# Performance work log

Measured on AMD Instinct MI355X. Metric: run time of the kernel, lower is better.

Reference implementation:

```python
import jax, jax.numpy as jnp
import numpy as np

N_NODES = 100000
N_EDGES = 1600000
N_FEAT = 128
HIDDEN = 128
N_CLASSES = 40


def gcn_conv(x, W, b, src, dst, norm, n):
    # PyG GCNConv: linear (no bias) -> gather src -> scale by sym norm -> scatter-add to dst -> + bias
    h = x @ W                      # [N, out]
    m = h[src] * norm[:, None]     # [E+N, out] gathered, normalized messages
    out = jax.ops.segment_sum(m, dst, num_segments=n)
    return out + b


def setup_inputs() -> dict:
    key = jax.random.key(0)
    ks = jax.random.split(key, 10)
    x = jax.random.normal(ks[0], (N_NODES, N_FEAT), dtype=jnp.float32)
    edge_index = jax.random.randint(ks[1], (2, N_EDGES), 0, N_NODES, dtype=jnp.int32)

    def lin(k, fan_in, fan_out):
        s = 1.0 / np.sqrt(fan_in)
        return (jax.random.uniform(k, (fan_in, fan_out), jnp.float32, -s, s))

    return {
        "x": x,
        "edge_index": edge_index,
        "W1": lin(ks[2], N_FEAT, HIDDEN), "b1": jnp.zeros((HIDDEN,), jnp.float32),
        "W2": lin(ks[3], HIDDEN, HIDDEN), "b2": jnp.zeros((HIDDEN,), jnp.float32),
        "W3": lin(ks[4], HIDDEN, HIDDEN), "b3": jnp.zeros((HIDDEN,), jnp.float32),
        "W4": lin(ks[5], HIDDEN, N_CLASSES), "b4": jnp.zeros((N_CLASSES,), jnp.float32),
    }


def reference(x, edge_index, W1, b1, W2, b2, W3, b3, W4, b4):
    n = x.shape[0]
    # add self-loops (PyG GCNConv default)
    loops = jnp.arange(n, dtype=edge_index.dtype)
    src = jnp.concatenate([edge_index[0], loops])
    dst = jnp.concatenate([edge_index[1], loops])
    # symmetric degree normalization: deg computed on destination index
    deg = jax.ops.segment_sum(jnp.ones_like(dst, x.dtype), dst, num_segments=n)
    dinv = jnp.where(deg > 0, jax.lax.rsqrt(deg), 0.0)
    norm = dinv[src] * dinv[dst]

    h = jax.nn.relu(gcn_conv(x, W1, b1, src, dst, norm, n))   # dropout = identity (eval)
    h = jax.nn.relu(gcn_conv(h, W2, b2, src, dst, norm, n))
    h = jax.nn.relu(gcn_conv(h, W3, b3, src, dst, norm, n))
    x_latent = h
    out = gcn_conv(h, W4, b4, src, dst, norm, n)
    return out, x_latent
```

## Files before the change

### kernel.cpp

```cpp
#include <hip/hip_runtime.h>
#include <hip/hip_bf16.h>
#include <hip/hip_fp16.h>


#define N_NODES 100000
#define N_EDGES 1600000

#define BSHIFT 7
#define BWIDTH 128
#define CELL_CAP 512
#define P1_EPT 16
#define P1_CHUNK 4096

typedef short s16x8 __attribute__((ext_vector_type(8)));
typedef _Float16 f16x8 __attribute__((ext_vector_type(8)));
typedef float f32x4 __attribute__((ext_vector_type(4)));
typedef float f32x2 __attribute__((ext_vector_type(2)));


__global__ __launch_bounds__(256) void pass1_bucket(const int* __restrict__ src,
                                                    const int* __restrict__ dst,
                                                    int* __restrict__ bcur2,
                                                    int2* __restrict__ cells,
                                                    int2* __restrict__ spill,
                                                    int* __restrict__ spillCnt,
                                                    int nb, int e) {
    __shared__ int hist[1024];
    __shared__ int base[1024];
    int t = threadIdx.x;
    int x = blockIdx.x & 7;
    int e0 = blockIdx.x * P1_CHUNK;

    for (int i = t; i < nb; i += 256) hist[i] = 0;
    __syncthreads();

    int ds[P1_EPT], ss[P1_EPT];
#pragma unroll
    for (int j = 0; j < P1_EPT; j++) {
        int i = e0 + j * 256 + t;
        if (i < e) {
            ds[j] = dst[i];
            ss[j] = src[i];
            atomicAdd(&hist[ds[j] >> BSHIFT], 1);
        } else {
            ds[j] = -1;
        }
    }
    __syncthreads();

    for (int i = t; i < nb; i += 256) {
        int h = hist[i];
        base[i] = (h > 0) ? atomicAdd(&bcur2[i * 8 + x], h) : 0;
        hist[i] = 0;
    }
    __syncthreads();

#pragma unroll
    for (int j = 0; j < P1_EPT; j++) {
        if (ds[j] >= 0) {
            int b = ds[j] >> BSHIFT;
            int r = atomicAdd(&hist[b], 1);
            int slot = base[b] + r;
            if (slot < CELL_CAP) {
                cells[(size_t)(b * 8 + x) * CELL_CAP + slot] = make_int2(ss[j], ds[j]);
            } else {
                int sp = atomicAdd(spillCnt, 1);
                spill[sp] = make_int2(ss[j], ds[j]);
            }
        }
    }
}

__global__ __launch_bounds__(256) void count_cells(const int* __restrict__ bcur2,
                                                   const int2* __restrict__ cells,
                                                   const int2* __restrict__ spill,
                                                   const int* __restrict__ spillCnt,
                                                   int* __restrict__ counts,
                                                   float* __restrict__ dinv,
                                                   int n) {
    __shared__ int cnt[BWIDTH];
    int b = blockIdx.x;
    int t = threadIdx.x;
    int nodeBase = b << BSHIFT;
    if (t < BWIDTH) cnt[t] = 0;
    __syncthreads();
    for (int x = 0; x < 8; x++) {
        int c = bcur2[b * 8 + x];
        if (c > CELL_CAP) c = CELL_CAP;
        const int2* cp = cells + (size_t)(b * 8 + x) * CELL_CAP;
        for (int s = t; s < c; s += 256) {
            atomicAdd(&cnt[cp[s].y - nodeBase], 1);
        }
    }
    int sc = *spillCnt;
    for (int s = t; s < sc; s += 256) {
        int d = spill[s].y;
        if ((d >> BSHIFT) == b) atomicAdd(&cnt[d - nodeBase], 1);
    }
    __syncthreads();
    if (t < BWIDTH) {
        int node = nodeBase + t;
        if (node < n) {
            int deg = cnt[t] + 1;
            counts[node] = deg;
            dinv[node] = 1.0f / sqrtf((float)deg);
        }
    }
}

__global__ __launch_bounds__(256) void scan_phase1(const int* __restrict__ counts,
                                                   int* __restrict__ blockSums, int n) {
    __shared__ int red[256];
    int t = threadIdx.x;
    int base = blockIdx.x * 1024 + t * 4;
    int s = 0;
    if (base + 3 < n) {
        int4 v = *(const int4*)(counts + base);
        s = ((v.x + 2) & ~3) + ((v.y + 2) & ~3) + ((v.z + 2) & ~3) + ((v.w + 2) & ~3);
    } else {
        for (int j = 0; j < 4; j++) if (base + j < n) s += (counts[base + j] + 2) & ~3;
    }
    red[t] = s;
    __syncthreads();
    for (int off = 128; off > 0; off >>= 1) {
        if (t < off) red[t] += red[t + off];
        __syncthreads();
    }
    if (t == 0) blockSums[blockIdx.x] = red[0];
}

__global__ __launch_bounds__(1024) void scan_phase2(int* __restrict__ blockSums, int nb) {
    __shared__ int sh[1024];
    int t = threadIdx.x;
    sh[t] = (t < nb) ? blockSums[t] : 0;
    __syncthreads();
    for (int off = 1; off < 1024; off <<= 1) {
        int v = (t >= off) ? sh[t - off] : 0;
        __syncthreads();
        sh[t] += v;
        __syncthreads();
    }
    if (t < nb) blockSums[t] = (t == 0) ? 0 : sh[t - 1];
}

__global__ __launch_bounds__(256) void scan_phase3(const int* __restrict__ counts,
                                                   const int* __restrict__ blockSums,
                                                   int* __restrict__ offsets, int n) {
    __shared__ int red[256];
    int t = threadIdx.x;
    int base = blockIdx.x * 1024 + t * 4;
    int c[4];
#pragma unroll
    for (int j = 0; j < 4; j++) c[j] = (base + j < n) ? ((counts[base + j] + 2) & ~3) : 0;
    int s = c[0] + c[1] + c[2] + c[3];
    red[t] = s;
    __syncthreads();
    for (int off = 1; off < 256; off <<= 1) {
        int v = (t >= off) ? red[t - off] : 0;
        __syncthreads();
        red[t] += v;
        __syncthreads();
    }
    int prefix = blockSums[blockIdx.x] + ((t == 0) ? 0 : red[t - 1]);
#pragma unroll
    for (int j = 0; j < 4; j++) {
        if (base + j < n) offsets[base + j] = prefix;
        prefix += c[j];
        if (base + j == n - 1) offsets[n] = prefix;
    }
}

__global__ __launch_bounds__(256) void pass2_scatter(const int* __restrict__ bcur2,
                                                     const int2* __restrict__ cells,
                                                     const int2* __restrict__ spill,
                                                     const int* __restrict__ spillCnt,
                                                     const int* __restrict__ offsets,
                                                     int* __restrict__ srcSorted, int n) {
    __shared__ int cur[BWIDTH];
    int b = blockIdx.x;
    int t = threadIdx.x;
    int nodeBase = b << BSHIFT;
    if (t < BWIDTH) cur[t] = 0;
    __syncthreads();
    for (int x = 0; x < 8; x++) {
        int c = bcur2[b * 8 + x];
        if (c > CELL_CAP) c = CELL_CAP;
        const int2* cp = cells + (size_t)(b * 8 + x) * CELL_CAP;
        for (int s = t; s < c; s += 256) {
            int2 p = cp[s];
            int r = atomicAdd(&cur[p.y - nodeBase], 1);
            srcSorted[offsets[p.y] + r] = p.x;
        }
    }
    int sc = *spillCnt;
    for (int s = t; s < sc; s += 256) {
        int2 p = spill[s];
        if ((p.y >> BSHIFT) == b) {
            int r = atomicAdd(&cur[p.y - nodeBase], 1);
            srcSorted[offsets[p.y] + r] = p.x;
        }
    }
    __syncthreads();
    if (t < BWIDTH) {
        int node = nodeBase + t;
        if (node < n) {
            int beg = offsets[node] + cur[t];
            int end = offsets[node + 1];
            for (int k = beg; k < end; k++) srcSorted[k] = n;
        }
    }
}


__device__ inline void split_bf16(float f, unsigned short& h, unsigned short& l) {
    unsigned u = __float_as_uint(f);
    unsigned hr = (u + 0x7FFFu + ((u >> 16) & 1u)) >> 16;
    h = (unsigned short)hr;
    float r = f - __uint_as_float(hr << 16);
    unsigned v = __float_as_uint(r);
    unsigned lr = (v + 0x7FFFu + ((v >> 16) & 1u)) >> 16;
    l = (unsigned short)lr;
}

__global__ __launch_bounds__(256) void prep_wfrag(const float* __restrict__ W,
                                                  short* __restrict__ wh,
                                                  short* __restrict__ wl,
                                                  __half* __restrict__ zrow) {
    if (zrow != nullptr && blockIdx.x == 0 && threadIdx.x < 64) {
        ((__half2*)zrow)[threadIdx.x] = __floats2half2_rn(0.f, 0.f);
    }
    int idx = blockIdx.x * 256 + threadIdx.x;
    int j    = idx & 7;
    int lane = (idx >> 3) & 63;
    int c    = (idx >> 9) & 3;
    int t    = idx >> 11;
    int quad = lane >> 4;
    int n = (t << 4) | (lane & 15);
    int k = (c << 5) + (quad << 3) + j;
    unsigned short h, l;
    split_bf16(W[k * 128 + n], h, l);
    wh[idx] = (short)h;
    wl[idx] = (short)l;
}

__global__ __launch_bounds__(256) void prep_wfrag16(const float* __restrict__ W,
                                                    _Float16* __restrict__ wh,
                                                    _Float16* __restrict__ wl,
                                                    __half* __restrict__ zrow) {
    if (zrow != nullptr && blockIdx.x == 0 && threadIdx.x < 64) {
        ((__half2*)zrow)[threadIdx.x] = __floats2half2_rn(0.f, 0.f);
    }
    int idx = blockIdx.x * 256 + threadIdx.x;
    int j    = idx & 7;
    int lane = (idx >> 3) & 63;
    int c    = (idx >> 9) & 3;
    int t    = idx >> 11;
    int quad = lane >> 4;
    int n = (t << 4) | (lane & 15);
    int k = (c << 5) + (quad << 3) + j;
    float v = W[k * 128 + n];
    _Float16 h = (_Float16)v;
    _Float16 l = (_Float16)((v - (float)h) * 2048.0f);
    wh[idx] = h;
    wl[idx] = l;
}

__global__ __launch_bounds__(256) void prep_wfrag40(const float* __restrict__ W,
                                                    _Float16* __restrict__ wh,
                                                    _Float16* __restrict__ wl) {
    int idx = blockIdx.x * 256 + threadIdx.x;
    int j    = idx & 7;
    int lane = (idx >> 3) & 63;
    int c    = (idx >> 9) & 3;
    int t    = idx >> 11;
    int quad = lane >> 4;
    int n = (t << 4) | (lane & 15);
    int k = (c << 5) + (quad << 3) + j;
    float v = (n < 40) ? W[k * 40 + n] : 0.f;
    _Float16 h = (_Float16)v;
    _Float16 l = (_Float16)((v - (float)h) * 2048.0f);
    wh[idx] = h;
    wl[idx] = l;
}


#define GEMM_GX 512

__global__ __launch_bounds__(256) void gemm_mfma(const float* __restrict__ A,
                                                 const short* __restrict__ wh,
                                                 const short* __restrict__ wl,
                                                 const float* __restrict__ dinv,
                                                 __half* __restrict__ C, int M) {
    int wv   = threadIdx.x >> 6;
    int lane = threadIdx.x & 63;
    int quad = lane >> 4;
    int mm   = lane & 15;
    int tbase = blockIdx.y * 4;

    s16x8 whf[4][4], wlf[4][4];
#pragma unroll
    for (int tt = 0; tt < 4; tt++)
#pragma unroll
        for (int c = 0; c < 4; c++) {
            int base = ((((tbase + tt) << 2) + c) << 6 | lane) << 3;
            whf[tt][c] = *(const s16x8*)(wh + base);
            wlf[tt][c] = *(const s16x8*)(wl + base);
        }

    int nStrips = M >> 4;
    for (int s = blockIdx.x * 4 + wv; s < nStrips; s += GEMM_GX * 4) {
        const float* ap = A + (size_t)((s << 4) + mm) * 128 + (quad << 3);
        f32x4 acc[4];
#pragma unroll
        for (int tt = 0; tt < 4; tt++) acc[tt] = (f32x4){0.f, 0.f, 0.f, 0.f};

#pragma unroll
        for (int c = 0; c < 4; c++) {
            float av[8];
            *(float4*)&av[0] = *(const float4*)(ap + (c << 5));
            *(float4*)&av[4] = *(const float4*)(ap + (c << 5) + 4);
            union { s16x8 v; unsigned short u[8]; } ah, al;
#pragma unroll
            for (int j = 0; j < 8; j++) split_bf16(av[j], ah.u[j], al.u[j]);
#pragma unroll
            for (int tt = 0; tt < 4; tt++) {
                acc[tt] = __builtin_amdgcn_mfma_f32_16x16x32_bf16(ah.v, whf[tt][c], acc[tt], 0, 0, 0);
                acc[tt] = __builtin_amdgcn_mfma_f32_16x16x32_bf16(ah.v, wlf[tt][c], acc[tt], 0, 0, 0);
                acc[tt] = __builtin_amdgcn_mfma_f32_16x16x32_bf16(al.v, whf[tt][c], acc[tt], 0, 0, 0);
                acc[tt] = __builtin_amdgcn_mfma_f32_16x16x32_bf16(al.v, wlf[tt][c], acc[tt], 0, 0, 0);
            }
        }
        int rbase = (s << 4) + (quad << 2);
        float dv[4];
#pragma unroll
        for (int r = 0; r < 4; r++) dv[r] = dinv[rbase + r];
        __half* cp = C + (size_t)rbase * 128 + (tbase << 4) + mm;
#pragma unroll
        for (int tt = 0; tt < 4; tt++) {
#pragma unroll
            for (int r = 0; r < 4; r++) {
                cp[(size_t)r * 128 + (tt << 4)] = __float2half(acc[tt][r] * dv[r]);
            }
        }
    }
}


__device__ inline f32x2 h2f(__half2 v) {
    float2 t = __half22float2(v);
    return (f32x2){t.x, t.y};
}

#define GATHER_NODE(NODE_ON, IDX, END)                                          \
    {                                                                           \
        int4 sA, sB;                                                            \
        bool have8 = (IDX + 8 <= END);                                          \
        if (have8) {                                                            \
            sA = *(const int4*)(srcSorted + IDX);                               \
            sB = *(const int4*)(srcSorted + IDX + 4);                           \
        }                                                                       \
        while (have8) {                                                         \
            int4 cA = sA, cB = sB;                                              \
            int nidx = IDX + 8;                                                 \
            bool nxt = (nidx + 8 <= END);                                       \
            if (nxt) {                                                          \
                sA = *(const int4*)(srcSorted + nidx);                          \
                sB = *(const int4*)(srcSorted + nidx + 4);                      \
            }                                                                   \
            __half2 v0 = *(const __half2*)(hb + (unsigned)cA.x * 256u + fb);    \
            __half2 v1 = *(const __half2*)(hb + (unsigned)cA.y * 256u + fb);    \
            __half2 v2 = *(const __half2*)(hb + (unsigned)cA.z * 256u + fb);    \
            __half2 v3 = *(const __half2*)(hb + (unsigned)cA.w * 256u + fb);    \
            __half2 v4 = *(const __half2*)(hb + (unsigned)cB.x * 256u + fb);    \
            __half2 v5 = *(const __half2*)(hb + (unsigned)cB.y * 256u + fb);    \
            __half2 v6 = *(const __half2*)(hb + (unsigned)cB.z * 256u + fb);    \
            __half2 v7 = *(const __half2*)(hb + (unsigned)cB.w * 256u + fb);    \
            a0 += h2f(v0); a1 += h2f(v1); a2 += h2f(v2); a3 += h2f(v3);         \
            a0 += h2f(v4); a1 += h2f(v5); a2 += h2f(v6); a3 += h2f(v7);         \
            IDX = nidx;                                                         \
            have8 = nxt;                                                        \
        }                                                                       \
        if (IDX + 4 <= END) {                                                   \
            int4 cA = *(const int4*)(srcSorted + IDX);                          \
            __half2 v0 = *(const __half2*)(hb + (unsigned)cA.x * 256u + fb);    \
            __half2 v1 = *(const __half2*)(hb + (unsigned)cA.y * 256u + fb);    \
            __half2 v2 = *(const __half2*)(hb + (unsigned)cA.z * 256u + fb);    \
            __half2 v3 = *(const __half2*)(hb + (unsigned)cA.w * 256u + fb);    \
            a0 += h2f(v0); a1 += h2f(v1); a2 += h2f(v2); a3 += h2f(v3);         \
        }                                                                       \
    }

__global__ __launch_bounds__(256) void fused_agg_gemm128(const __half* __restrict__ hsrc,
                                                         const _Float16* __restrict__ wh,
                                                         const _Float16* __restrict__ wl,
                                                         const float* __restrict__ dinv,
                                                         const int* __restrict__ offsets,
                                                         const int* __restrict__ srcSorted,
                                                         const float* __restrict__ bias,
                                                         __half* __restrict__ hdst, int n) {
    __shared__ __align__(16) _Float16 aST[16 * 136];
    int wave = threadIdx.x >> 6;
    int lane = threadIdx.x & 63;
    int strip = blockIdx.x;
    int f = lane * 2;
    unsigned fb = (unsigned)f * 2u;
    const char* hb = (const char*)hsrc;
    float2 bv = *(const float2*)(bias + f);

    for (int i = 0; i < 4; i++) {
        int row = (wave << 2) + i;
        int node = (strip << 4) + row;
        bool on = (node < n);
        float di = on ? dinv[node] : 0.f;
        int idx = on ? offsets[node] : 0;
        int end = on ? offsets[node + 1] : 0;

        f32x2 z = (f32x2){0.f, 0.f};
        f32x2 a0 = z, a1 = z, a2 = z, a3 = z;
        if (on) a0 = h2f(*(const __half2*)(hb + (unsigned)node * 256u + fb));
        GATHER_NODE(on, idx, end);

        f32x2 s = (a0 + a1) + (a2 + a3);
        float ox = fmaxf(di * s.x + bv.x, 0.f);
        float oy = fmaxf(di * s.y + bv.y, 0.f);
        *(__half2*)(aST + row * 136 + f) = __floats2half2_rn(ox, oy);
    }
    __syncthreads();

    int quad = lane >> 4;
    int mm   = lane & 15;
    f16x8 av[4];
#pragma unroll
    for (int c = 0; c < 4; c++)
        av[c] = *(const f16x8*)(aST + mm * 136 + (c << 5) + (quad << 3));
    int rbase = (strip << 4) + (quad << 2);
    float dv[4];
#pragma unroll
    for (int r = 0; r < 4; r++) dv[r] = (rbase + r < n) ? dinv[rbase + r] : 0.f;

#pragma unroll
    for (int t2 = 0; t2 < 2; t2++) {
        int gt = (wave << 1) + t2;
        f32x4 acch = (f32x4){0.f, 0.f, 0.f, 0.f};
        f32x4 accl = (f32x4){0.f, 0.f, 0.f, 0.f};
#pragma unroll
        for (int c = 0; c < 4; c++) {
            int base = (((gt << 2) + c) << 6 | lane) << 3;
            f16x8 bh = *(const f16x8*)(wh + base);
            f16x8 bl = *(const f16x8*)(wl + base);
            acch = __builtin_amdgcn_mfma_f32_16x16x32_f16(av[c], bh, acch, 0, 0, 0);
            accl = __builtin_amdgcn_mfma_f32_16x16x32_f16(av[c], bl, accl, 0, 0, 0);
        }
#pragma unroll
        for (int r = 0; r < 4; r++) {
            if (rbase + r < n) {
                float v = acch[r] + accl[r] * (1.0f / 2048.0f);
                hdst[(size_t)(rbase + r) * 128 + (gt << 4) + mm] = __float2half(v * dv[r]);
            }
        }
    }
}

__global__ __launch_bounds__(256) void fused_agg_gemm40(const __half* __restrict__ hsrc,
                                                        const _Float16* __restrict__ wh,
                                                        const _Float16* __restrict__ wl,
                                                        const float* __restrict__ dinv,
                                                        const int* __restrict__ offsets,
                                                        const int* __restrict__ srcSorted,
                                                        const float* __restrict__ bias,
                                                        float* __restrict__ xlat,
                                                        __half* __restrict__ hdst, int n) {
    __shared__ __align__(16) _Float16 aST[16 * 136];
    int wave = threadIdx.x >> 6;
    int lane = threadIdx.x & 63;
    int strip = blockIdx.x;
    int f = lane * 2;
    unsigned fb = (unsigned)f * 2u;
    const char* hb = (const char*)hsrc;
    float2 bv = *(const float2*)(bias + f);

    if (blockIdx.x == 0 && threadIdx.x < 20) {
        ((__half2*)(hdst + (size_t)n * 40))[threadIdx.x] = __floats2half2_rn(0.f, 0.f);
    }

    for (int i = 0; i < 4; i++) {
        int row = (wave << 2) + i;
        int node = (strip << 4) + row;
        bool on = (node < n);
        float di = on ? dinv[node] : 0.f;
        int idx = on ? offsets[node] : 0;
        int end = on ? offsets[node + 1] : 0;

        f32x2 z = (f32x2){0.f, 0.f};
        f32x2 a0 = z, a1 = z, a2 = z, a3 = z;
        if (on) a0 = h2f(*(const __half2*)(hb + (unsigned)node * 256u + fb));
        GATHER_NODE(on, idx, end);

        f32x2 s = (a0 + a1) + (a2 + a3);
        float ox = fmaxf(di * s.x + bv.x, 0.f);
        float oy = fmaxf(di * s.y + bv.y, 0.f);
        if (on) *(float2*)(xlat + (size_t)node * 128 + f) = make_float2(ox, oy);
        *(__half2*)(aST + row * 136 + f) = __floats2half2_rn(ox, oy);
    }
    __syncthreads();

    if (wave < 3) {
        int quad = lane >> 4;
        int mm   = lane & 15;
        f16x8 av[4];
#pragma unroll
        for (int c = 0; c < 4; c++)
            av[c] = *(const f16x8*)(aST + mm * 136 + (c << 5) + (quad << 3));
        int rbase = (strip << 4) + (quad << 2);
        float dv[4];
#pragma unroll
        for (int r = 0; r < 4; r++) dv[r] = (rbase + r < n) ? dinv[rbase + r] : 0.f;

        int gt = wave;
        f32x4 acch = (f32x4){0.f, 0.f, 0.f, 0.f};
        f32x4 accl = (f32x4){0.f, 0.f, 0.f, 0.f};
#pragma unroll
        for (int c = 0; c < 4; c++) {
            int base = (((gt << 2) + c) << 6 | lane) << 3;
            f16x8 bh = *(const f16x8*)(wh + base);
            f16x8 bl = *(const f16x8*)(wl + base);
            acch = __builtin_amdgcn_mfma_f32_16x16x32_f16(av[c], bh, acch, 0, 0, 0);
            accl = __builtin_amdgcn_mfma_f32_16x16x32_f16(av[c], bl, accl, 0, 0, 0);
        }
        int col = (gt << 4) + mm;
#pragma unroll
        for (int r = 0; r < 4; r++) {
            if (rbase + r < n && col < 40) {
                float v = acch[r] + accl[r] * (1.0f / 2048.0f);
                hdst[(size_t)(rbase + r) * 40 + col] = __float2half(v * dv[r]);
            }
        }
    }
}

__global__ __launch_bounds__(256) void agg40_tri(const __half* __restrict__ h,
                                                 const float* __restrict__ dinv,
                                                 const int* __restrict__ offsets,
                                                 const int* __restrict__ srcSorted,
                                                 const float* __restrict__ bias,
                                                 float* __restrict__ out, int n) {
    int wave = threadIdx.x >> 6;
    int lane = threadIdx.x & 63;
    unsigned sub = (unsigned)lane / 20u;
    int fi = lane - (int)sub * 20;
    bool act = (sub < 3u);
    int f = fi * 2;
    unsigned fb = (unsigned)fi * 4u;
    const char* hb = (const char*)h;
    float bx = act ? bias[f] : 0.f;
    float by = act ? bias[f + 1] : 0.f;
    int ntri = (n + 2) / 3;

    for (int p = blockIdx.x * 4 + wave; p < ntri; p += gridDim.x * 4) {
        int node = p * 3 + (int)sub;
        bool on = act && (node < n);
        float di = on ? dinv[node] : 0.f;
        int idx = on ? offsets[node] : 0;
        int end = on ? offsets[node + 1] : 0;

        f32x2 z = (f32x2){0.f, 0.f};
        f32x2 a0 = z, a1 = z, a2 = z, a3 = z;
        if (on) a0 = h2f(*(const __half2*)(hb + (unsigned)node * 80u + fb));

        while (__any(idx + 8 <= end)) {
            bool c = (idx + 8 <= end);
            if (c) {
                int4 sA = *(const int4*)(srcSorted + idx);
                int4 sB = *(const int4*)(srcSorted + idx + 4);
                a0 += h2f(*(const __half2*)(hb + (unsigned)sA.x * 80u + fb));
                a1 += h2f(*(const __half2*)(hb + (unsigned)sA.y * 80u + fb));
                a2 += h2f(*(const __half2*)(hb + (unsigned)sA.z * 80u + fb));
                a3 += h2f(*(const __half2*)(hb + (unsigned)sA.w * 80u + fb));
                a0 += h2f(*(const __half2*)(hb + (unsigned)sB.x * 80u + fb));
                a1 += h2f(*(const __half2*)(hb + (unsigned)sB.y * 80u + fb));
                a2 += h2f(*(const __half2*)(hb + (unsigned)sB.z * 80u + fb));
                a3 += h2f(*(const __half2*)(hb + (unsigned)sB.w * 80u + fb));
                idx += 8;
            }
        }
        if (idx + 4 <= end) {
            int4 sA = *(const int4*)(srcSorted + idx);
            a0 += h2f(*(const __half2*)(hb + (unsigned)sA.x * 80u + fb));
            a1 += h2f(*(const __half2*)(hb + (unsigned)sA.y * 80u + fb));
            a2 += h2f(*(const __half2*)(hb + (unsigned)sA.z * 80u + fb));
            a3 += h2f(*(const __half2*)(hb + (unsigned)sA.w * 80u + fb));
        }

        if (on) {
            f32x2 s = (a0 + a1) + (a2 + a3);
            float ox = di * s.x + bx;
            float oy = di * s.y + by;
            *(float2*)(out + (size_t)node * 40 + f) = make_float2(ox, oy);
        }
    }
}


extern "C" void kernel_launch(void* const* d_in, const int* in_sizes, int n_in,
                              void* d_out, int out_size, void* d_ws, size_t ws_size,
                              hipStream_t stream) {
    const float* x  = (const float*)d_in[0];
    const int* edge = (const int*)d_in[1];
    const float* W1 = (const float*)d_in[2]; const float* b1 = (const float*)d_in[3];
    const float* W2 = (const float*)d_in[4]; const float* b2 = (const float*)d_in[5];
    const float* W3 = (const float*)d_in[6]; const float* b3 = (const float*)d_in[7];
    const float* W4 = (const float*)d_in[8]; const float* b4 = (const float*)d_in[9];

    const int N = in_sizes[0] / 128;
    const int E = in_sizes[1] / 2;
    const int* src = edge;
    const int* dst = edge + E;

    float* out_final = (float*)d_out;
    float* x_latent  = (float*)d_out + (size_t)N * 40;

    const int nbk = (N + BWIDTH - 1) >> BSHIFT;

    char* w = (char*)d_ws;
    int* counts    = (int*)w;  w += (size_t)N * 4;
    int* offsets   = (int*)w;  w += (size_t)(N + 4) * 4;
    float* dinv    = (float*)w; w += (size_t)N * 4;
    int* srcSorted = (int*)w;  w += (size_t)(E + 4 * N) * 4;
    int* blockSums = (int*)w;  w += (size_t)1024 * 4;
    int* bcur2     = (int*)w;  w += (size_t)8448 * 4;
    int* spillCnt  = (int*)w;  w += (size_t)64 * 4;
    short* wfrag   = (short*)w;    w += (size_t)2 * 16384 * 2;
    _Float16* wf16 = (_Float16*)w; w += (size_t)4 * 16384 * 2;
    _Float16* wf40 = (_Float16*)w; w += (size_t)2 * 6144 * 2;
    w = (char*)(((uintptr_t)w + 255) & ~(uintptr_t)255);
    __half* hA   = (__half*)w; w += (size_t)(N + 1) * 128 * 2;
    __half* hB16 = (__half*)w; w += (size_t)(N + 1) * 128 * 2;

    int2* cells = (int2*)hA;
    int2* spill = cells + (size_t)nbk * 8 * CELL_CAP;

    short* wh1 = wfrag;            short* wl1 = wfrag + 16384;
    _Float16* wh2 = wf16;          _Float16* wl2 = wf16 + 16384;
    _Float16* wh3 = wf16 + 32768;  _Float16* wl3 = wf16 + 49152;
    _Float16* wh4 = wf40;          _Float16* wl4 = wf40 + 6144;

    int nb = (N + 1023) / 1024;
    int p1b = (E + P1_CHUNK - 1) / P1_CHUNK;
    int nStrips = (N + 15) / 16;

    hipMemsetAsync(bcur2, 0, (size_t)(8448 + 64) * 4, stream);
    pass1_bucket<<<p1b, 256, 0, stream>>>(src, dst, bcur2, cells, spill, spillCnt, nbk, E);
    count_cells<<<nbk, 256, 0, stream>>>(bcur2, cells, spill, spillCnt, counts, dinv, N);
    scan_phase1<<<nb, 256, 0, stream>>>(counts, blockSums, N);
    scan_phase2<<<1, 1024, 0, stream>>>(blockSums, nb);
    scan_phase3<<<nb, 256, 0, stream>>>(counts, blockSums, offsets, N);
    pass2_scatter<<<nbk, 256, 0, stream>>>(bcur2, cells, spill, spillCnt, offsets, srcSorted, N);

    prep_wfrag<<<64, 256, 0, stream>>>(W1, wh1, wl1, hA + (size_t)N * 128);
    prep_wfrag16<<<64, 256, 0, stream>>>(W2, wh2, wl2, hB16 + (size_t)N * 128);
    prep_wfrag16<<<64, 256, 0, stream>>>(W3, wh3, wl3, nullptr);
    prep_wfrag40<<<24, 256, 0, stream>>>(W4, wh4, wl4);

    dim3 gGemm(GEMM_GX, 2);

    gemm_mfma<<<gGemm, 256, 0, stream>>>(x, wh1, wl1, dinv, hA, N);
    fused_agg_gemm128<<<nStrips, 256, 0, stream>>>(hA, wh2, wl2, dinv, offsets,
                                                   srcSorted, b1, hB16, N);
    fused_agg_gemm128<<<nStrips, 256, 0, stream>>>(hB16, wh3, wl3, dinv, offsets,
                                                   srcSorted, b2, hA, N);
    fused_agg_gemm40<<<nStrips, 256, 0, stream>>>(hA, wh4, wl4, dinv, offsets,
                                                  srcSorted, b3, x_latent, hB16, N);
    agg40_tri<<<2048, 256, 0, stream>>>(hB16, dinv, offsets, srcSorted, b4, out_final, N);
}
```

Baseline: 450.9 us.

## Degree-sort nodes for balanced aggregation strips and pack bucket cells to 32-bit

Result: slower. 1.048 ms (+132.4%).

```diff
diff --git a/kernel.cpp b/kernel.cpp
--- a/kernel.cpp
+++ b/kernel.cpp
@@ -21,7 +21,7 @@
 __global__ __launch_bounds__(256) void pass1_bucket(const int* __restrict__ src,
                                                     const int* __restrict__ dst,
                                                     int* __restrict__ bcur2,
-                                                    int2* __restrict__ cells,
+                                                    unsigned* __restrict__ cells,
                                                     int2* __restrict__ spill,
                                                     int* __restrict__ spillCnt,
                                                     int nb, int e) {
@@ -62,7 +62,8 @@
             int r = atomicAdd(&hist[b], 1);
             int slot = base[b] + r;
             if (slot < CELL_CAP) {
-                cells[(size_t)(b * 8 + x) * CELL_CAP + slot] = make_int2(ss[j], ds[j]);
+                cells[(size_t)(b * 8 + x) * CELL_CAP + slot] =
+                    ((unsigned)(ds[j] & (BWIDTH - 1)) << 25) | (unsigned)ss[j];
             } else {
                 int sp = atomicAdd(spillCnt, 1);
                 spill[sp] = make_int2(ss[j], ds[j]);
@@ -72,7 +73,7 @@
 }
 
 __global__ __launch_bounds__(256) void count_cells(const int* __restrict__ bcur2,
-                                                   const int2* __restrict__ cells,
+                                                   const unsigned* __restrict__ cells,
                                                    const int2* __restrict__ spill,
                                                    const int* __restrict__ spillCnt,
                                                    int* __restrict__ counts,
@@ -87,9 +88,9 @@
     for (int x = 0; x < 8; x++) {
         int c = bcur2[b * 8 + x];
         if (c > CELL_CAP) c = CELL_CAP;
-        const int2* cp = cells + (size_t)(b * 8 + x) * CELL_CAP;
+        const unsigned* cp = cells + (size_t)(b * 8 + x) * CELL_CAP;
         for (int s = t; s < c; s += 256) {
-            atomicAdd(&cnt[cp[s].y - nodeBase], 1);
+            atomicAdd(&cnt[cp[s] >> 25], 1);
         }
     }
     int sc = *spillCnt;
@@ -171,7 +172,7 @@
 }
 
 __global__ __launch_bounds__(256) void pass2_scatter(const int* __restrict__ bcur2,
-                                                     const int2* __restrict__ cells,
+                                                     const unsigned* __restrict__ cells,
                                                      const int2* __restrict__ spill,
                                                      const int* __restrict__ spillCnt,
                                                      const int* __restrict__ offsets,
@@ -185,11 +186,12 @@
     for (int x = 0; x < 8; x++) {
         int c = bcur2[b * 8 + x];
         if (c > CELL_CAP) c = CELL_CAP;
-        const int2* cp = cells + (size_t)(b * 8 + x) * CELL_CAP;
+        const unsigned* cp = cells + (size_t)(b * 8 + x) * CELL_CAP;
         for (int s = t; s < c; s += 256) {
-            int2 p = cp[s];
-            int r = atomicAdd(&cur[p.y - nodeBase], 1);
-            srcSorted[offsets[p.y] + r] = p.x;
+            unsigned v = cp[s];
+            int l = (int)(v >> 25);
+            int r = atomicAdd(&cur[l], 1);
+            srcSorted[offsets[nodeBase + l] + r] = (int)(v & 0x1FFFFFFu);
         }
     }
     int sc = *spillCnt;
@@ -208,6 +210,38 @@
             int end = offsets[node + 1];
             for (int k = beg; k < end; k++) srcSorted[k] = n;
         }
+    }
+}
+
+
+__global__ void sort_hist(const int* __restrict__ counts, int* __restrict__ hist, int n) {
+    __shared__ int lh[64];
+    int t = threadIdx.x;
+    if (t < 64) lh[t] = 0;
+    __syncthreads();
+    int i = blockIdx.x * 256 + t;
+    if (i < n) {
+        int b = (counts[i] + 2) >> 2; if (b > 63) b = 63;
+        atomicAdd(&lh[b], 1);
+    }
+    __syncthreads();
+    if (t < 64 && lh[t] > 0) atomicAdd(&hist[t], lh[t]);
+}
+
+__global__ void sort_scan64(int* __restrict__ hist) {
+    if (threadIdx.x == 0 && blockIdx.x == 0) {
+        int acc = 0;
+        for (int i = 0; i < 64; i++) { int v = hist[i]; hist[i] = acc; acc += v; }
+    }
+}
+
+__global__ void sort_scatter(const int* __restrict__ counts, int* __restrict__ hist,
+                             int* __restrict__ perm, int n) {
+    int i = blockIdx.x * blockDim.x + threadIdx.x;
+    if (i < n) {
+        int b = (counts[i] + 2) >> 2; if (b > 63) b = 63;
+        int pos = atomicAdd(&hist[b], 1);
+        perm[pos] = i;
     }
 }
 
@@ -351,7 +385,7 @@
     return (f32x2){t.x, t.y};
 }
 
-#define GATHER_NODE(NODE_ON, IDX, END)                                          \
+#define GATHER_NODE(IDX, END)                                                   \
     {                                                                           \
         int4 sA, sB;                                                            \
         bool have8 = (IDX + 8 <= END);                                          \
@@ -396,6 +430,7 @@
                                                          const float* __restrict__ dinv,
                                                          const int* __restrict__ offsets,
                                                          const int* __restrict__ srcSorted,
+                                                         const int* __restrict__ perm,
                                                          const float* __restrict__ bias,
                                                          __half* __restrict__ hdst, int n) {
     __shared__ __align__(16) _Float16 aST[16 * 136];
@@ -409,8 +444,9 @@
 
     for (int i = 0; i < 4; i++) {
         int row = (wave << 2) + i;
-        int node = (strip << 4) + row;
-        bool on = (node < n);
+        int k = (strip << 4) + row;
+        bool on = (k < n);
+        int node = on ? perm[k] : 0;
         float di = on ? dinv[node] : 0.f;
         int idx = on ? offsets[node] : 0;
         int end = on ? offsets[node + 1] : 0;
@@ -418,7 +454,7 @@
         f32x2 z = (f32x2){0.f, 0.f};
         f32x2 a0 = z, a1 = z, a2 = z, a3 = z;
         if (on) a0 = h2f(*(const __half2*)(hb + (unsigned)node * 256u + fb));
-        GATHER_NODE(on, idx, end);
+        GATHER_NODE(idx, end);
 
         f32x2 s = (a0 + a1) + (a2 + a3);
         float ox = fmaxf(di * s.x + bv.x, 0.f);
@@ -433,10 +469,14 @@
 #pragma unroll
     for (int c = 0; c < 4; c++)
         av[c] = *(const f16x8*)(aST + mm * 136 + (c << 5) + (quad << 3));
-    int rbase = (strip << 4) + (quad << 2);
-    float dv[4];
-#pragma unroll
-    for (int r = 0; r < 4; r++) dv[r] = (rbase + r < n) ? dinv[rbase + r] : 0.f;
+    int kb = (strip << 4) + (quad << 2);
+    int nd[4]; float dv[4];
+#pragma unroll
+    for (int r = 0; r < 4; r++) {
+        bool v = (kb + r < n);
+        nd[r] = v ? perm[kb + r] : 0;
+        dv[r] = v ? dinv[nd[r]] : 0.f;
+    }
 
 #pragma unroll
     for (int t2 = 0; t2 < 2; t2++) {
@@ -453,9 +493,9 @@
         }
 #pragma unroll
         for (int r = 0; r < 4; r++) {
-            if (rbase + r < n) {
+            if (kb + r < n) {
                 float v = acch[r] + accl[r] * (1.0f / 2048.0f);
-                hdst[(size_t)(rbase + r) * 128 + (gt << 4) + mm] = __float2half(v * dv[r]);
+                hdst[(size_t)nd[r] * 128 + (gt << 4) + mm] = __float2half(v * dv[r]);
             }
         }
     }
@@ -467,6 +507,7 @@
                                                         const float* __restrict__ dinv,
                                                         const int* __restrict__ offsets,
                                                         const int* __restrict__ srcSorted,
+                                                        const int* __restrict__ perm,
                                                         const float* __restrict__ bias,
                                                         float* __restrict__ xlat,
                                                         __half* __restrict__ hdst, int n) {
@@ -483,10 +524,13 @@
         ((__half2*)(hdst + (size_t)n * 40))[threadIdx.x] = __floats2half2_rn(0.f, 0.f);
     }
 
+    int ndg[4];
     for (int i = 0; i < 4; i++) {
         int row = (wave << 2) + i;
-        int node = (strip << 4) + row;
-        bool on = (node < n);
+        int k = (strip << 4) + row;
+        bool on = (k < n);
+        int node = on ? perm[k] : 0;
+        ndg[i] = node;
         float di = on ? dinv[node] : 0.f;
         int idx = on ? offsets[node] : 0;
         int end = on ? offsets[node + 1] : 0;
@@ -494,7 +538,7 @@
         f32x2 z = (f32x2){0.f, 0.f};
         f32x2 a0 = z, a1 = z, a2 = z, a3 = z;
         if (on) a0 = h2f(*(const __half2*)(hb + (unsigned)node * 256u + fb));
-        GATHER_NODE(on, idx, end);
+        GATHER_NODE(idx, end);
 
         f32x2 s = (a0 + a1) + (a2 + a3);
         float ox = fmaxf(di * s.x + bv.x, 0.f);
@@ -511,10 +555,14 @@
 #pragma unroll
         for (int c = 0; c < 4; c++)
             av[c] = *(const f16x8*)(aST + mm * 136 + (c << 5) + (quad << 3));
-        int rbase = (strip << 4) + (quad << 2);
-        float dv[4];
-#pragma unroll
-        for (int r = 0; r < 4; r++) dv[r] = (rbase + r < n) ? dinv[rbase + r] : 0.f;
+        int kb = (strip << 4) + (quad << 2);
+        int nd[4]; float dv[4];
+#pragma unroll
+        for (int r = 0; r < 4; r++) {
+            bool v = (kb + r < n);
+            nd[r] = v ? perm[kb + r] : 0;
+            dv[r] = v ? dinv[nd[r]] : 0.f;
+        }
 
         int gt = wave;
         f32x4 acch = (f32x4){0.f, 0.f, 0.f, 0.f};
@@ -530,9 +578,9 @@
         int col = (gt << 4) + mm;
 #pragma unroll
         for (int r = 0; r < 4; r++) {
-            if (rbase + r < n && col < 40) {
+            if (kb + r < n && col < 40) {
                 float v = acch[r] + accl[r] * (1.0f / 2048.0f);
-                hdst[(size_t)(rbase + r) * 40 + col] = __float2half(v * dv[r]);
+                hdst[(size_t)nd[r] * 40 + col] = __float2half(v * dv[r]);
             }
         }
     }
@@ -625,10 +673,12 @@
     int* counts    = (int*)w;  w += (size_t)N * 4;
     int* offsets   = (int*)w;  w += (size_t)(N + 4) * 4;
     float* dinv    = (float*)w; w += (size_t)N * 4;
+    int* perm      = (int*)w;  w += (size_t)N * 4;
     int* srcSorted = (int*)w;  w += (size_t)(E + 4 * N) * 4;
     int* blockSums = (int*)w;  w += (size_t)1024 * 4;
     int* bcur2     = (int*)w;  w += (size_t)8448 * 4;
     int* spillCnt  = (int*)w;  w += (size_t)64 * 4;
+    int* sortHist  = (int*)w;  w += (size_t)128 * 4;
     short* wfrag   = (short*)w;    w += (size_t)2 * 16384 * 2;
     _Float16* wf16 = (_Float16*)w; w += (size_t)4 * 16384 * 2;
     _Float16* wf40 = (_Float16*)w; w += (size_t)2 * 6144 * 2;
@@ -636,25 +686,29 @@
     __half* hA   = (__half*)w; w += (size_t)(N + 1) * 128 * 2;
     __half* hB16 = (__half*)w; w += (size_t)(N + 1) * 128 * 2;
 
-    int2* cells = (int2*)hA;
-    int2* spill = cells + (size_t)nbk * 8 * CELL_CAP;
+    unsigned* cells = (unsigned*)hA;
+    int2* spill = (int2*)(cells + (size_t)nbk * 8 * CELL_CAP);
 
     short* wh1 = wfrag;            short* wl1 = wfrag + 16384;
     _Float16* wh2 = wf16;          _Float16* wl2 = wf16 + 16384;
     _Float16* wh3 = wf16 + 32768;  _Float16* wl3 = wf16 + 49152;
     _Float16* wh4 = wf40;          _Float16* wl4 = wf40 + 6144;
 
+    int gN = (N + 255) / 256;
     int nb = (N + 1023) / 1024;
     int p1b = (E + P1_CHUNK - 1) / P1_CHUNK;
     int nStrips = (N + 15) / 16;
 
-    hipMemsetAsync(bcur2, 0, (size_t)(8448 + 64) * 4, stream);
+    hipMemsetAsync(bcur2, 0, (size_t)(8448 + 64 + 128) * 4, stream);
     pass1_bucket<<<p1b, 256, 0, stream>>>(src, dst, bcur2, cells, spill, spillCnt, nbk, E);
     count_cells<<<nbk, 256, 0, stream>>>(bcur2, cells, spill, spillCnt, counts, dinv, N);
     scan_phase1<<<nb, 256, 0, stream>>>(counts, blockSums, N);
     scan_phase2<<<1, 1024, 0, stream>>>(blockSums, nb);
     scan_phase3<<<nb, 256, 0, stream>>>(counts, blockSums, offsets, N);
     pass2_scatter<<<nbk, 256, 0, stream>>>(bcur2, cells, spill, spillCnt, offsets, srcSorted, N);
+    sort_hist<<<gN, 256, 0, stream>>>(counts, sortHist, N);
+    sort_scan64<<<1, 64, 0, stream>>>(sortHist);
+    sort_scatter<<<gN, 256, 0, stream>>>(counts, sortHist, perm, N);
 
     prep_wfrag<<<64, 256, 0, stream>>>(W1, wh1, wl1, hA + (size_t)N * 128);
     prep_wfrag16<<<64, 256, 0, stream>>>(W2, wh2, wl2, hB16 + (size_t)N * 128);
@@ -665,10 +719,10 @@
 
     gemm_mfma<<<gGemm, 256, 0, stream>>>(x, wh1, wl1, dinv, hA, N);
     fused_agg_gemm128<<<nStrips, 256, 0, stream>>>(hA, wh2, wl2, dinv, offsets,
-                                                   srcSorted, b1, hB16, N);
+                                                   srcSorted, perm, b1, hB16, N);
     fused_agg_gemm128<<<nStrips, 256, 0, stream>>>(hB16, wh3, wl3, dinv, offsets,
-                                                   srcSorted, b2, hA, N);
+                                                   srcSorted, perm, b2, hA, N);
     fused_agg_gemm40<<<nStrips, 256, 0, stream>>>(hA, wh4, wl4, dinv, offsets,
-                                                  srcSorted, b3, x_latent, hB16, N);
+                                                  srcSorted, perm, b3, x_latent, hB16, N);
     agg40_tri<<<2048, 256, 0, stream>>>(hB16, dinv, offsets, srcSorted, b4, out_final, N);
 }
```
